# Kernel optimization log

Hardware: AMD Instinct MI355X
Metric: run time of the kernel (lower is better)

Reference implementation:

```python
import jax, jax.numpy as jnp
import numpy as np

N_NODES = 100000
N_EDGES = 1600000
N_GRAPHS = 256
F_NODE, F_EDGE, HID, OUT = 64, 16, 128, 128
BN_SCALE = 1.0 / np.sqrt(1.0 + 1e-5)  # BatchNorm eval with running mean 0, var 1


def setup_inputs() -> dict:
    key = jax.random.key(0)
    ks = iter(jax.random.split(key, 64))
    inp = {}
    inp["x"] = jax.random.normal(next(ks), (N_NODES, F_NODE), dtype=jnp.float32)
    inp["edge_attr"] = jax.random.normal(next(ks), (N_EDGES, F_EDGE), dtype=jnp.float32)
    inp["edge_index"] = jax.random.randint(next(ks), (2, N_EDGES), 0, N_NODES)
    inp["batch"] = jnp.sort(jax.random.randint(next(ks), (N_NODES,), 0, N_GRAPHS))

    def p(shape, scale):
        return (jax.random.normal(next(ks), shape, dtype=jnp.float32) * scale)

    in_dims = [F_NODE, HID, HID]
    for i, d in enumerate(in_dims):
        inp[f"el_w{i}"] = p((F_EDGE, d), F_EDGE ** -0.5)
        inp[f"el_b{i}"] = jnp.zeros((d,), jnp.float32)
        inp[f"c{i}_w1"] = p((d, HID), d ** -0.5)
        inp[f"c{i}_b1"] = jnp.zeros((HID,), jnp.float32)
        inp[f"c{i}_g"] = jnp.ones((HID,), jnp.float32)
        inp[f"c{i}_bt"] = jnp.zeros((HID,), jnp.float32)
        inp[f"c{i}_w2"] = p((HID, HID), HID ** -0.5)
        inp[f"c{i}_b2"] = jnp.zeros((HID,), jnp.float32)
    inp["o_w1"] = p((HID, OUT), HID ** -0.5)
    inp["o_b1"] = jnp.zeros((OUT,), jnp.float32)
    inp["o_w2"] = p((OUT, OUT), OUT ** -0.5)
    inp["o_b2"] = jnp.zeros((OUT,), jnp.float32)
    return inp


def reference(x, edge_attr,
              el_w0, el_b0, c0_w1, c0_b1, c0_g, c0_bt, c0_w2, c0_b2,
              el_w1, el_b1, c1_w1, c1_b1, c1_g, c1_bt, c1_w2, c1_b2,
              el_w2, el_b2, c2_w1, c2_b1, c2_g, c2_bt, c2_w2, c2_b2,
              o_w1, o_b1, o_w2, o_b2,
              edge_index, batch):
    src, dst = edge_index[0], edge_index[1]
    n = x.shape[0]
    layers = [
        (el_w0, el_b0, c0_w1, c0_b1, c0_g, c0_bt, c0_w2, c0_b2),
        (el_w1, el_b1, c1_w1, c1_b1, c1_g, c1_bt, c1_w2, c1_b2),
        (el_w2, el_b2, c2_w1, c2_b1, c2_g, c2_bt, c2_w2, c2_b2),
    ]
    h = x
    for (ew, eb, w1, b1, g, bt, w2, b2) in layers:
        ea = edge_attr @ ew + eb                              # [E, d]
        msg = jax.nn.relu(h[src] + ea)                        # GINEConv message
        agg = jax.ops.segment_sum(msg, dst, num_segments=n)   # scatter-sum to targets
        hh = h + agg                                          # (1+eps)*x + aggr, eps=0
        hh = hh @ w1 + b1                                     # MLP: Linear
        hh = g * (hh * BN_SCALE) + bt                         # BatchNorm1d (eval)
        hh = jax.nn.relu(hh)
        hh = hh @ w2 + b2                                     # MLP: Linear
        h = jax.nn.relu(hh)                                   # dropout(p=0, eval) + act
    s = jax.ops.segment_sum(h, batch, num_segments=N_GRAPHS)
    cnt = jax.ops.segment_sum(jnp.ones((n,), h.dtype), batch, num_segments=N_GRAPHS)
    pooled = s / jnp.maximum(cnt, 1.0)[:, None]               # scatter-mean pooling
    out = jax.nn.relu(pooled @ o_w1 + o_b1) @ o_w2 + o_b2     # out_lin
    return out
```

## Files before the change

### kernel.cpp

```cpp
#include <hip/hip_runtime.h>
#include <hip/hip_fp16.h>
#include <cstdint>
#include <cstddef>

#define N_NODES_C  100000
#define N_EDGES_C  1600000
#define N_GRAPHS_C 256
#define HID_C      128
#define BN_SCALE_C 0.9999950000374997f

#define SCAN_B 1024
#define SCAN_NB ((N_NODES_C + SCAN_B - 1) / SCAN_B)

typedef _Float16 h8 __attribute__((ext_vector_type(8)));
typedef _Float16 h4 __attribute__((ext_vector_type(4)));
typedef float    f4 __attribute__((ext_vector_type(4)));

struct __align__(16) H8 { __half2 v[4]; };
struct __align__(8)  Hq { __half2 a, b; };

__global__ __launch_bounds__(256) void hist_kernel(
    const int* __restrict__ dst, int* __restrict__ counts, int n_edges)
{
    int e = blockIdx.x * 256 + threadIdx.x;
    if (e < n_edges) atomicAdd(&counts[dst[e]], 1);
}

__global__ __launch_bounds__(SCAN_B) void scan1_kernel(
    const int* __restrict__ counts, int* __restrict__ incl,
    int* __restrict__ blocksums, int n)
{
    __shared__ int sdata[SCAN_B];
    const int lid = threadIdx.x;
    const int i = blockIdx.x * SCAN_B + lid;
    sdata[lid] = (i < n) ? counts[i] : 0;
    __syncthreads();
#pragma unroll
    for (int off = 1; off < SCAN_B; off <<= 1) {
        int t = (lid >= off) ? sdata[lid - off] : 0;
        __syncthreads();
        sdata[lid] += t;
        __syncthreads();
    }
    if (i < n) incl[i] = sdata[lid];
    if (lid == SCAN_B - 1) blocksums[blockIdx.x] = sdata[lid];
}

__global__ void scan2_kernel(const int* __restrict__ blocksums,
                             int* __restrict__ blockoffs, int nb)
{
    if (threadIdx.x == 0 && blockIdx.x == 0) {
        int off = 0;
        for (int b = 0; b < nb; ++b) { blockoffs[b] = off; off += blocksums[b]; }
    }
}

__global__ __launch_bounds__(SCAN_B) void scan3_kernel(
    int* __restrict__ incl, const int* __restrict__ blockoffs, int n)
{
    const int i = blockIdx.x * SCAN_B + threadIdx.x;
    if (i < n) incl[i] += blockoffs[blockIdx.x];
}

__global__ __launch_bounds__(256) void initrows_kernel(
    const int* __restrict__ incl, const int* __restrict__ counts,
    int* __restrict__ rowstart, int* __restrict__ cursor, int n)
{
    const int i = blockIdx.x * 256 + threadIdx.x;
    if (i < n) {
        const int rs = incl[i] - counts[i];
        rowstart[i] = rs;
        cursor[i]   = rs;
    }
}

__global__ __launch_bounds__(256) void scatter_kernel(
    const int* __restrict__ src, const int* __restrict__ dst,
    int* __restrict__ cursor, int* __restrict__ perm_src,
    int* __restrict__ perm_eid, int n_edges)
{
    const int e = blockIdx.x * 256 + threadIdx.x;
    if (e < n_edges) {
        const int pos = atomicAdd(&cursor[dst[e]], 1);
        perm_src[pos] = src[e];
        perm_eid[pos] = e;
    }
}

__global__ __launch_bounds__(256) void permute_ea_f16_kernel(
    const float* __restrict__ edge_attr, const int* __restrict__ perm_eid,
    __half* __restrict__ ea_f16, int n_edges)
{
    const int j = blockIdx.x * 256 + threadIdx.x;
    if (j >= n_edges) return;
    const int eid = perm_eid[j];
    const float4* p = (const float4*)(edge_attr + (size_t)eid * 16);
    const float4 q0 = p[0], q1 = p[1], q2 = p[2], q3 = p[3];
    H8 a, b;
    a.v[0] = __floats2half2_rn(q0.x, q0.y);
    a.v[1] = __floats2half2_rn(q0.z, q0.w);
    a.v[2] = __floats2half2_rn(q1.x, q1.y);
    a.v[3] = __floats2half2_rn(q1.z, q1.w);
    b.v[0] = __floats2half2_rn(q2.x, q2.y);
    b.v[1] = __floats2half2_rn(q2.z, q2.w);
    b.v[2] = __floats2half2_rn(q3.x, q3.y);
    b.v[3] = __floats2half2_rn(q3.z, q3.w);
    H8* o = (H8*)(ea_f16 + (size_t)j * 16);
    o[0] = a;
    o[1] = b;
}

__global__ __launch_bounds__(256) void cast_f16_kernel(
    const float* __restrict__ in, _Float16* __restrict__ out, int n4)
{
    const int i = blockIdx.x * 256 + threadIdx.x;
    if (i >= n4) return;
    const float4 v = ((const float4*)in)[i];
    h4 o; o[0] = (_Float16)v.x; o[1] = (_Float16)v.y;
    o[2] = (_Float16)v.z; o[3] = (_Float16)v.w;
    *(h4*)(out + (size_t)i * 4) = o;
}

__global__ __launch_bounds__(256) void transpose_w_kernel(
    const float* __restrict__ w, _Float16* __restrict__ wt, int K, int N)
{
    const int i = blockIdx.x * 256 + threadIdx.x;
    if (i >= K * N) return;
    const int n = i / K;
    const int k = i - n * K;
    wt[(size_t)n * K + k] = (_Float16)w[(size_t)k * N + n];
}

__device__ __forceinline__ float4 eamlp_f16(const H8* __restrict__ p,
                                            const __half2 (*ew2)[4],
                                            const float4 ebv)
{
    const H8 a = p[0], b = p[1];
    __half2 c0 = {0.f, 0.f}, c1 = {0.f, 0.f}, c2 = {0.f, 0.f}, c3 = {0.f, 0.f};
#pragma unroll
    for (int k2 = 0; k2 < 4; ++k2) {
        c0 = __hfma2(a.v[k2], ew2[k2][0], c0);
        c1 = __hfma2(a.v[k2], ew2[k2][1], c1);
        c2 = __hfma2(a.v[k2], ew2[k2][2], c2);
        c3 = __hfma2(a.v[k2], ew2[k2][3], c3);
    }
#pragma unroll
    for (int k2 = 0; k2 < 4; ++k2) {
        c0 = __hfma2(b.v[k2], ew2[4 + k2][0], c0);
        c1 = __hfma2(b.v[k2], ew2[4 + k2][1], c1);
        c2 = __hfma2(b.v[k2], ew2[4 + k2][2], c2);
        c3 = __hfma2(b.v[k2], ew2[4 + k2][3], c3);
    }
    float4 m;
    m.x = ebv.x + __low2float(c0) + __high2float(c0);
    m.y = ebv.y + __low2float(c1) + __high2float(c1);
    m.z = ebv.z + __low2float(c2) + __high2float(c2);
    m.w = ebv.w + __low2float(c3) + __high2float(c3);
    return m;
}

template<int DIN>
__global__ __launch_bounds__(256) void gine_agg_kernel(
    const __half* __restrict__ h16, const __half* __restrict__ ea_f16,
    const int* __restrict__ perm_src,
    const int* __restrict__ rowstart, const int* __restrict__ rowend,
    const float* __restrict__ ew, const float* __restrict__ eb,
    float* __restrict__ agg, int n_nodes)
{
    constexpr int NQ    = DIN / 4;
    constexpr int SLOTS = 256 / NQ;
    const int fq   = threadIdx.x & (NQ - 1);
    const int slot = threadIdx.x / NQ;
    const int v = blockIdx.x * SLOTS + slot;
    if (v >= n_nodes) return;

    __half2 ew2[8][4];
#pragma unroll
    for (int k2 = 0; k2 < 8; ++k2)
#pragma unroll
        for (int fi = 0; fi < 4; ++fi)
            ew2[k2][fi] = __floats2half2_rn(ew[(size_t)(2 * k2)     * DIN + fq * 4 + fi],
                                            ew[(size_t)(2 * k2 + 1) * DIN + fq * 4 + fi]);
    const float4 ebv = *(const float4*)(eb + fq * 4);

    const int s0 = rowstart[v];
    const int s1 = rowend[v];

    float4 acc = {0.f, 0.f, 0.f, 0.f};
    int j = s0;
    for (; j + 2 <= s1; j += 2) {
        const int sn0 = perm_src[j + 0];
        const int sn1 = perm_src[j + 1];
        const Hq hq0 = *(const Hq*)(h16 + (size_t)sn0 * DIN + fq * 4);
        const Hq hq1 = *(const Hq*)(h16 + (size_t)sn1 * DIN + fq * 4);
        const H8* p0 = (const H8*)(ea_f16 + (size_t)(j + 0) * 16);
        const H8* p1 = (const H8*)(ea_f16 + (size_t)(j + 1) * 16);
        const float4 m0 = eamlp_f16(p0, ew2, ebv);
        const float4 m1 = eamlp_f16(p1, ew2, ebv);
        const float2 l0 = __half22float2(hq0.a), u0 = __half22float2(hq0.b);
        const float2 l1 = __half22float2(hq1.a), u1 = __half22float2(hq1.b);
        acc.x += fmaxf(m0.x + l0.x, 0.f) + fmaxf(m1.x + l1.x, 0.f);
        acc.y += fmaxf(m0.y + l0.y, 0.f) + fmaxf(m1.y + l1.y, 0.f);
        acc.z += fmaxf(m0.z + u0.x, 0.f) + fmaxf(m1.z + u1.x, 0.f);
        acc.w += fmaxf(m0.w + u0.y, 0.f) + fmaxf(m1.w + u1.y, 0.f);
    }
    if (j < s1) {
        const int sn = perm_src[j];
        const Hq hq = *(const Hq*)(h16 + (size_t)sn * DIN + fq * 4);
        const H8* p = (const H8*)(ea_f16 + (size_t)j * 16);
        const float4 m = eamlp_f16(p, ew2, ebv);
        const float2 l = __half22float2(hq.a), u = __half22float2(hq.b);
        acc.x += fmaxf(m.x + l.x, 0.f);
        acc.y += fmaxf(m.y + l.y, 0.f);
        acc.z += fmaxf(m.z + u.x, 0.f);
        acc.w += fmaxf(m.w + u.y, 0.f);
    }
    *(float4*)(agg + (size_t)v * DIN + fq * 4) = acc;
}

template<int DIN>
__global__ __launch_bounds__(256) void node_mfma_kernel(
    const float* __restrict__ h, const float* __restrict__ agg,
    const _Float16* __restrict__ w1t, const float* __restrict__ b1,
    const float* __restrict__ gm, const float* __restrict__ bt,
    const _Float16* __restrict__ w2t, const float* __restrict__ b2,
    float* __restrict__ hout, _Float16* __restrict__ h16out, int n_tiles)
{
    constexpr int SXP = DIN + 8;
    constexpr int STP = HID_C + 8;
    __shared__ _Float16 s_x[4][16][SXP];
    __shared__ _Float16 s_t[4][16][STP];

    const int w    = threadIdx.x >> 6;
    const int lane = threadIdx.x & 63;
    int tile = blockIdx.x * 4 + w;
    if (tile >= n_tiles) tile = n_tiles - 1;
    const int node0 = tile * 16;

    constexpr int KQ = DIN / 4;
    for (int it = lane; it < 16 * KQ; it += 64) {
        const int ni = it / KQ;
        const int k4 = (it - ni * KQ) * 4;
        const float4 hv = *(const float4*)(h   + (size_t)(node0 + ni) * DIN + k4);
        const float4 av = *(const float4*)(agg + (size_t)(node0 + ni) * DIN + k4);
        h4 o;
        o[0] = (_Float16)(hv.x + av.x);
        o[1] = (_Float16)(hv.y + av.y);
        o[2] = (_Float16)(hv.z + av.z);
        o[3] = (_Float16)(hv.w + av.w);
        *(h4*)&s_x[w][ni][k4] = o;
    }
    __syncthreads();

    const int ln   = lane & 15;
    const int quad = lane >> 4;

#pragma unroll
    for (int nt = 0; nt < 8; ++nt) {
        const int col = nt * 16 + ln;
        const float bv = b1[col];
        f4 acc = {bv, bv, bv, bv};
#pragma unroll
        for (int ks = 0; ks < DIN / 32; ++ks) {
            const h8 af = *(const h8*)&s_x[w][ln][ks * 32 + quad * 8];
            const h8 bf = *(const h8*)(w1t + (size_t)col * DIN + ks * 32 + quad * 8);
            acc = __builtin_amdgcn_mfma_f32_16x16x32_f16(af, bf, acc, 0, 0, 0);
        }
        const float gv = gm[col], btv = bt[col];
#pragma unroll
        for (int r = 0; r < 4; ++r) {
            const float t = fmaxf(fmaf(acc[r] * BN_SCALE_C, gv, btv), 0.f);
            s_t[w][quad * 4 + r][col] = (_Float16)t;
        }
    }
    __syncthreads();

#pragma unroll
    for (int nt = 0; nt < 8; ++nt) {
        const int col = nt * 16 + ln;
        const float bv = b2[col];
        f4 acc = {bv, bv, bv, bv};
#pragma unroll
        for (int ks = 0; ks < HID_C / 32; ++ks) {
            const h8 af = *(const h8*)&s_t[w][ln][ks * 32 + quad * 8];
            const h8 bf = *(const h8*)(w2t + (size_t)col * HID_C + ks * 32 + quad * 8);
            acc = __builtin_amdgcn_mfma_f32_16x16x32_f16(af, bf, acc, 0, 0, 0);
        }
#pragma unroll
        for (int r = 0; r < 4; ++r) {
            const int node = node0 + quad * 4 + r;
            const float v = fmaxf(acc[r], 0.f);
            hout[(size_t)node * HID_C + col] = v;
            h16out[(size_t)node * HID_C + col] = (_Float16)v;
        }
    }
}

__global__ __launch_bounds__(256) void pool_kernel(
    const float* __restrict__ hfin, const int* __restrict__ batch,
    const float* __restrict__ w1, const float* __restrict__ b1,
    const float* __restrict__ w2, const float* __restrict__ b2,
    float* __restrict__ out, int n_nodes)
{
    const int gid = blockIdx.x;

    int lo = 0, hi = n_nodes;
    while (lo < hi) { int mid = (lo + hi) >> 1; if (batch[mid] < gid) lo = mid + 1; else hi = mid; }
    const int start = lo;
    hi = n_nodes;
    while (lo < hi) { int mid = (lo + hi) >> 1; if (batch[mid] < gid + 1) lo = mid + 1; else hi = mid; }
    const int end = lo;

    const int f = threadIdx.x & (HID_C - 1);
    const int half = threadIdx.x >> 7;

    float sum = 0.f;
    for (int n = start + half; n < end; n += 2)
        sum += hfin[(size_t)n * HID_C + f];

    __shared__ float s_sum[2][HID_C];
    __shared__ float s_p[HID_C];
    __shared__ float s_t[HID_C];
    s_sum[half][f] = sum;
    __syncthreads();

    if (threadIdx.x < HID_C) {
        const float cnt = (float)(end - start);
        s_p[f] = (s_sum[0][f] + s_sum[1][f]) / fmaxf(cnt, 1.f);
    }
    __syncthreads();

    if (threadIdx.x < HID_C) {
        float acc = b1[f];
        for (int k = 0; k < HID_C; ++k) acc = fmaf(s_p[k], w1[k * HID_C + f], acc);
        s_t[f] = fmaxf(acc, 0.f);
    }
    __syncthreads();

    if (threadIdx.x < HID_C) {
        float acc = b2[f];
        for (int k = 0; k < HID_C; ++k) acc = fmaf(s_t[k], w2[k * HID_C + f], acc);
        out[(size_t)gid * HID_C + f] = acc;
    }
}

extern "C" void kernel_launch(void* const* d_in, const int* in_sizes, int n_in,
                              void* d_out, int out_size, void* d_ws, size_t ws_size,
                              hipStream_t stream)
{
    const float* x         = (const float*)d_in[0];
    const float* edge_attr = (const float*)d_in[1];
    const int*   edge_index= (const int*)  d_in[2];
    const int*   batch     = (const int*)  d_in[3];
    const int*   src = edge_index;
    const int*   dst = edge_index + N_EDGES_C;

    const float* el_w[3] = {(const float*)d_in[4],  (const float*)d_in[12], (const float*)d_in[20]};
    const float* el_b[3] = {(const float*)d_in[5],  (const float*)d_in[13], (const float*)d_in[21]};
    const float* c_w1[3] = {(const float*)d_in[6],  (const float*)d_in[14], (const float*)d_in[22]};
    const float* c_b1[3] = {(const float*)d_in[7],  (const float*)d_in[15], (const float*)d_in[23]};
    const float* c_g [3] = {(const float*)d_in[8],  (const float*)d_in[16], (const float*)d_in[24]};
    const float* c_bt[3] = {(const float*)d_in[9],  (const float*)d_in[17], (const float*)d_in[25]};
    const float* c_w2[3] = {(const float*)d_in[10], (const float*)d_in[18], (const float*)d_in[26]};
    const float* c_b2[3] = {(const float*)d_in[11], (const float*)d_in[19], (const float*)d_in[27]};
    const float* o_w1 = (const float*)d_in[28];
    const float* o_b1 = (const float*)d_in[29];
    const float* o_w2 = (const float*)d_in[30];
    const float* o_b2 = (const float*)d_in[31];

    char* wsp = (char*)d_ws;
    size_t used = 0;
    auto alloc = [&](size_t bytes) { char* p = wsp + used; used += (bytes + 255) & ~(size_t)255; return p; };
    float* h        = (float*)alloc((size_t)N_NODES_C * HID_C * 4);
    float* agg      = (float*)alloc((size_t)N_NODES_C * HID_C * 4);
    int*   counts   = (int*)alloc((size_t)N_NODES_C * 4);
    int*   incl     = (int*)alloc((size_t)N_NODES_C * 4);
    int*   rowstart = (int*)alloc((size_t)N_NODES_C * 4);
    int*   cursor   = (int*)alloc((size_t)N_NODES_C * 4);
    int*   blocksums= (int*)alloc(128 * 4);
    int*   blockoffs= (int*)alloc(128 * 4);
    int*   perm_src = (int*)alloc((size_t)N_EDGES_C * 4);
    int*   perm_eid = (int*)alloc((size_t)N_EDGES_C * 4);
    __half*    ea_f16 = (__half*)alloc((size_t)N_EDGES_C * 16 * 2);
    _Float16*  h_f16  = (_Float16*)alloc((size_t)N_NODES_C * HID_C * 2);
    _Float16*  x_f16  = (_Float16*)alloc((size_t)N_NODES_C * 64 * 2);
    _Float16*  w1t[3], *w2t[3];
    for (int l = 0; l < 3; ++l) {
        w1t[l] = (_Float16*)alloc((size_t)HID_C * HID_C * 2);
        w2t[l] = (_Float16*)alloc((size_t)HID_C * HID_C * 2);
    }
    (void)ws_size;

    hipMemsetAsync(counts, 0, (size_t)N_NODES_C * 4, stream);
    hist_kernel<<<(N_EDGES_C + 255) / 256, 256, 0, stream>>>(dst, counts, N_EDGES_C);
    scan1_kernel<<<SCAN_NB, SCAN_B, 0, stream>>>(counts, incl, blocksums, N_NODES_C);
    scan2_kernel<<<1, 64, 0, stream>>>(blocksums, blockoffs, SCAN_NB);
    scan3_kernel<<<SCAN_NB, SCAN_B, 0, stream>>>(incl, blockoffs, N_NODES_C);
    initrows_kernel<<<(N_NODES_C + 255) / 256, 256, 0, stream>>>(incl, counts, rowstart,
                                                                 cursor, N_NODES_C);
    scatter_kernel<<<(N_EDGES_C + 255) / 256, 256, 0, stream>>>(src, dst, cursor,
                                                                perm_src, perm_eid, N_EDGES_C);
    permute_ea_f16_kernel<<<(N_EDGES_C + 255) / 256, 256, 0, stream>>>(
        edge_attr, perm_eid, ea_f16, N_EDGES_C);
    cast_f16_kernel<<<(N_NODES_C * 64 / 4 + 255) / 256, 256, 0, stream>>>(
        x, x_f16, N_NODES_C * 64 / 4);
    for (int l = 0; l < 3; ++l) {
        const int K1 = (l == 0) ? 64 : HID_C;
        transpose_w_kernel<<<(K1 * HID_C + 255) / 256, 256, 0, stream>>>(
            c_w1[l], w1t[l], K1, HID_C);
        transpose_w_kernel<<<(HID_C * HID_C + 255) / 256, 256, 0, stream>>>(
            c_w2[l], w2t[l], HID_C, HID_C);
    }

    const int n_tiles = N_NODES_C / 16;
    const int nb_node = (n_tiles + 3) / 4;

    for (int l = 0; l < 3; ++l) {
        if (l == 0) {
            gine_agg_kernel<64><<<(N_NODES_C + 15) / 16, 256, 0, stream>>>(
                (const __half*)x_f16, ea_f16, perm_src, rowstart, incl,
                el_w[0], el_b[0], agg, N_NODES_C);
            node_mfma_kernel<64><<<nb_node, 256, 0, stream>>>(
                x, agg, w1t[0], c_b1[0], c_g[0], c_bt[0], w2t[0], c_b2[0],
                h, h_f16, n_tiles);
        } else {
            gine_agg_kernel<128><<<(N_NODES_C + 7) / 8, 256, 0, stream>>>(
                (const __half*)h_f16, ea_f16, perm_src, rowstart, incl,
                el_w[l], el_b[l], agg, N_NODES_C);
            node_mfma_kernel<128><<<nb_node, 256, 0, stream>>>(
                h, agg, w1t[l], c_b1[l], c_g[l], c_bt[l], w2t[l], c_b2[l],
                h, h_f16, n_tiles);
        }
    }

    pool_kernel<<<N_GRAPHS_C, 256, 0, stream>>>(h, batch, o_w1, o_b1, o_w2, o_b2,
                                                (float*)d_out, N_NODES_C);
}
```

Measured before the change: 1.104 ms.

## Fuse edge-attr permute into scatter, drop fp32 node state, half-precision edge MLP

```diff
diff --git a/kernel.cpp b/kernel.cpp
--- a/kernel.cpp
+++ b/kernel.cpp
@@ -14,10 +14,9 @@
 
 typedef _Float16 h8 __attribute__((ext_vector_type(8)));
 typedef _Float16 h4 __attribute__((ext_vector_type(4)));
+typedef _Float16 hv2 __attribute__((ext_vector_type(2)));
 typedef float    f4 __attribute__((ext_vector_type(4)));
-
-struct __align__(16) H8 { __half2 v[4]; };
-struct __align__(8)  Hq { __half2 a, b; };
+typedef float    f2 __attribute__((ext_vector_type(2)));
 
 __global__ __launch_bounds__(256) void hist_kernel(
     const int* __restrict__ dst, int* __restrict__ counts, int n_edges)
@@ -74,38 +73,28 @@
     }
 }
 
-__global__ __launch_bounds__(256) void scatter_kernel(
+__global__ __launch_bounds__(256) void scatter_fused_kernel(
     const int* __restrict__ src, const int* __restrict__ dst,
+    const float* __restrict__ edge_attr,
     int* __restrict__ cursor, int* __restrict__ perm_src,
-    int* __restrict__ perm_eid, int n_edges)
+    _Float16* __restrict__ ea_f16, int n_edges)
 {
     const int e = blockIdx.x * 256 + threadIdx.x;
-    if (e < n_edges) {
-        const int pos = atomicAdd(&cursor[dst[e]], 1);
-        perm_src[pos] = src[e];
-        perm_eid[pos] = e;
-    }
-}
-
-__global__ __launch_bounds__(256) void permute_ea_f16_kernel(
-    const float* __restrict__ edge_attr, const int* __restrict__ perm_eid,
-    __half* __restrict__ ea_f16, int n_edges)
-{
-    const int j = blockIdx.x * 256 + threadIdx.x;
-    if (j >= n_edges) return;
-    const int eid = perm_eid[j];
-    const float4* p = (const float4*)(edge_attr + (size_t)eid * 16);
+    if (e >= n_edges) return;
+    const int pos = atomicAdd(&cursor[dst[e]], 1);
+    perm_src[pos] = src[e];
+    const float4* p = (const float4*)(edge_attr + (size_t)e * 16);
     const float4 q0 = p[0], q1 = p[1], q2 = p[2], q3 = p[3];
-    H8 a, b;
-    a.v[0] = __floats2half2_rn(q0.x, q0.y);
-    a.v[1] = __floats2half2_rn(q0.z, q0.w);
-    a.v[2] = __floats2half2_rn(q1.x, q1.y);
-    a.v[3] = __floats2half2_rn(q1.z, q1.w);
-    b.v[0] = __floats2half2_rn(q2.x, q2.y);
-    b.v[1] = __floats2half2_rn(q2.z, q2.w);
-    b.v[2] = __floats2half2_rn(q3.x, q3.y);
-    b.v[3] = __floats2half2_rn(q3.z, q3.w);
-    H8* o = (H8*)(ea_f16 + (size_t)j * 16);
+    h8 a, b;
+    a[0] = (_Float16)q0.x; a[1] = (_Float16)q0.y;
+    a[2] = (_Float16)q0.z; a[3] = (_Float16)q0.w;
+    a[4] = (_Float16)q1.x; a[5] = (_Float16)q1.y;
+    a[6] = (_Float16)q1.z; a[7] = (_Float16)q1.w;
+    b[0] = (_Float16)q2.x; b[1] = (_Float16)q2.y;
+    b[2] = (_Float16)q2.z; b[3] = (_Float16)q2.w;
+    b[4] = (_Float16)q3.x; b[5] = (_Float16)q3.y;
+    b[6] = (_Float16)q3.z; b[7] = (_Float16)q3.w;
+    h8* o = (h8*)(ea_f16 + (size_t)pos * 16);
     o[0] = a;
     o[1] = b;
 }
@@ -131,37 +120,9 @@
     wt[(size_t)n * K + k] = (_Float16)w[(size_t)k * N + n];
 }
 
-__device__ __forceinline__ float4 eamlp_f16(const H8* __restrict__ p,
-                                            const __half2 (*ew2)[4],
-                                            const float4 ebv)
-{
-    const H8 a = p[0], b = p[1];
-    __half2 c0 = {0.f, 0.f}, c1 = {0.f, 0.f}, c2 = {0.f, 0.f}, c3 = {0.f, 0.f};
-#pragma unroll
-    for (int k2 = 0; k2 < 4; ++k2) {
-        c0 = __hfma2(a.v[k2], ew2[k2][0], c0);
-        c1 = __hfma2(a.v[k2], ew2[k2][1], c1);
-        c2 = __hfma2(a.v[k2], ew2[k2][2], c2);
-        c3 = __hfma2(a.v[k2], ew2[k2][3], c3);
-    }
-#pragma unroll
-    for (int k2 = 0; k2 < 4; ++k2) {
-        c0 = __hfma2(b.v[k2], ew2[4 + k2][0], c0);
-        c1 = __hfma2(b.v[k2], ew2[4 + k2][1], c1);
-        c2 = __hfma2(b.v[k2], ew2[4 + k2][2], c2);
-        c3 = __hfma2(b.v[k2], ew2[4 + k2][3], c3);
-    }
-    float4 m;
-    m.x = ebv.x + __low2float(c0) + __high2float(c0);
-    m.y = ebv.y + __low2float(c1) + __high2float(c1);
-    m.z = ebv.z + __low2float(c2) + __high2float(c2);
-    m.w = ebv.w + __low2float(c3) + __high2float(c3);
-    return m;
-}
-
 template<int DIN>
 __global__ __launch_bounds__(256) void gine_agg_kernel(
-    const __half* __restrict__ h16, const __half* __restrict__ ea_f16,
+    const _Float16* __restrict__ h16, const _Float16* __restrict__ ea_f16,
     const int* __restrict__ perm_src,
     const int* __restrict__ rowstart, const int* __restrict__ rowend,
     const float* __restrict__ ew, const float* __restrict__ eb,
@@ -174,57 +135,103 @@
     const int v = blockIdx.x * SLOTS + slot;
     if (v >= n_nodes) return;
 
-    __half2 ew2[8][4];
-#pragma unroll
-    for (int k2 = 0; k2 < 8; ++k2)
-#pragma unroll
-        for (int fi = 0; fi < 4; ++fi)
-            ew2[k2][fi] = __floats2half2_rn(ew[(size_t)(2 * k2)     * DIN + fq * 4 + fi],
-                                            ew[(size_t)(2 * k2 + 1) * DIN + fq * 4 + fi]);
-    const float4 ebv = *(const float4*)(eb + fq * 4);
+    hv2 ew01[16], ew23[16];
+#pragma unroll
+    for (int k = 0; k < 16; ++k) {
+        const float* wr = ew + (size_t)k * DIN + fq * 4;
+        ew01[k][0] = (_Float16)wr[0]; ew01[k][1] = (_Float16)wr[1];
+        ew23[k][0] = (_Float16)wr[2]; ew23[k][1] = (_Float16)wr[3];
+    }
+    hv2 eb01, eb23;
+    {
+        const float4 ebv = *(const float4*)(eb + fq * 4);
+        eb01[0] = (_Float16)ebv.x; eb01[1] = (_Float16)ebv.y;
+        eb23[0] = (_Float16)ebv.z; eb23[1] = (_Float16)ebv.w;
+    }
+    const hv2 zz = {(_Float16)0.f, (_Float16)0.f};
 
     const int s0 = rowstart[v];
     const int s1 = rowend[v];
 
-    float4 acc = {0.f, 0.f, 0.f, 0.f};
+    f4 acc = {0.f, 0.f, 0.f, 0.f};
     int j = s0;
     for (; j + 2 <= s1; j += 2) {
         const int sn0 = perm_src[j + 0];
         const int sn1 = perm_src[j + 1];
-        const Hq hq0 = *(const Hq*)(h16 + (size_t)sn0 * DIN + fq * 4);
-        const Hq hq1 = *(const Hq*)(h16 + (size_t)sn1 * DIN + fq * 4);
-        const H8* p0 = (const H8*)(ea_f16 + (size_t)(j + 0) * 16);
-        const H8* p1 = (const H8*)(ea_f16 + (size_t)(j + 1) * 16);
-        const float4 m0 = eamlp_f16(p0, ew2, ebv);
-        const float4 m1 = eamlp_f16(p1, ew2, ebv);
-        const float2 l0 = __half22float2(hq0.a), u0 = __half22float2(hq0.b);
-        const float2 l1 = __half22float2(hq1.a), u1 = __half22float2(hq1.b);
-        acc.x += fmaxf(m0.x + l0.x, 0.f) + fmaxf(m1.x + l1.x, 0.f);
-        acc.y += fmaxf(m0.y + l0.y, 0.f) + fmaxf(m1.y + l1.y, 0.f);
-        acc.z += fmaxf(m0.z + u0.x, 0.f) + fmaxf(m1.z + u1.x, 0.f);
-        acc.w += fmaxf(m0.w + u0.y, 0.f) + fmaxf(m1.w + u1.y, 0.f);
+        const h4 hq0 = *(const h4*)(h16 + (size_t)sn0 * DIN + fq * 4);
+        const h4 hq1 = *(const h4*)(h16 + (size_t)sn1 * DIN + fq * 4);
+        const h8* p0 = (const h8*)(ea_f16 + (size_t)(j + 0) * 16);
+        const h8* p1 = (const h8*)(ea_f16 + (size_t)(j + 1) * 16);
+        const h8 a0 = p0[0], a1 = p0[1];
+        const h8 b0 = p1[0], b1 = p1[1];
+
+        hv2 c01 = eb01, c23 = eb23;
+        hv2 d01 = eb01, d23 = eb23;
+#pragma unroll
+        for (int k = 0; k < 8; ++k) {
+            const hv2 ba = {a0[k], a0[k]};
+            const hv2 bb = {b0[k], b0[k]};
+            c01 += ba * ew01[k];  c23 += ba * ew23[k];
+            d01 += bb * ew01[k];  d23 += bb * ew23[k];
+        }
+#pragma unroll
+        for (int k = 0; k < 8; ++k) {
+            const hv2 ba = {a1[k], a1[k]};
+            const hv2 bb = {b1[k], b1[k]};
+            c01 += ba * ew01[8 + k];  c23 += ba * ew23[8 + k];
+            d01 += bb * ew01[8 + k];  d23 += bb * ew23[8 + k];
+        }
+        const hv2 h001 = {hq0[0], hq0[1]}, h023 = {hq0[2], hq0[3]};
+        const hv2 h101 = {hq1[0], hq1[1]}, h123 = {hq1[2], hq1[3]};
+        c01 = __builtin_elementwise_max(c01 + h001, zz);
+        c23 = __builtin_elementwise_max(c23 + h023, zz);
+        d01 = __builtin_elementwise_max(d01 + h101, zz);
+        d23 = __builtin_elementwise_max(d23 + h123, zz);
+        const f2 r0 = __builtin_convertvector(c01, f2);
+        const f2 r1 = __builtin_convertvector(c23, f2);
+        const f2 r2 = __builtin_convertvector(d01, f2);
+        const f2 r3 = __builtin_convertvector(d23, f2);
+        acc[0] += r0[0] + r2[0];
+        acc[1] += r0[1] + r2[1];
+        acc[2] += r1[0] + r3[0];
+        acc[3] += r1[1] + r3[1];
     }
     if (j < s1) {
         const int sn = perm_src[j];
-        const Hq hq = *(const Hq*)(h16 + (size_t)sn * DIN + fq * 4);
-        const H8* p = (const H8*)(ea_f16 + (size_t)j * 16);
-        const float4 m = eamlp_f16(p, ew2, ebv);
-        const float2 l = __half22float2(hq.a), u = __half22float2(hq.b);
-        acc.x += fmaxf(m.x + l.x, 0.f);
-        acc.y += fmaxf(m.y + l.y, 0.f);
-        acc.z += fmaxf(m.z + u.x, 0.f);
-        acc.w += fmaxf(m.w + u.y, 0.f);
-    }
-    *(float4*)(agg + (size_t)v * DIN + fq * 4) = acc;
+        const h4 hq = *(const h4*)(h16 + (size_t)sn * DIN + fq * 4);
+        const h8* p = (const h8*)(ea_f16 + (size_t)j * 16);
+        const h8 a0 = p[0], a1 = p[1];
+        hv2 c01 = eb01, c23 = eb23;
+#pragma unroll
+        for (int k = 0; k < 8; ++k) {
+            const hv2 ba = {a0[k], a0[k]};
+            c01 += ba * ew01[k];  c23 += ba * ew23[k];
+        }
+#pragma unroll
+        for (int k = 0; k < 8; ++k) {
+            const hv2 ba = {a1[k], a1[k]};
+            c01 += ba * ew01[8 + k];  c23 += ba * ew23[8 + k];
+        }
+        const hv2 h01 = {hq[0], hq[1]}, h23 = {hq[2], hq[3]};
+        c01 = __builtin_elementwise_max(c01 + h01, zz);
+        c23 = __builtin_elementwise_max(c23 + h23, zz);
+        const f2 r0 = __builtin_convertvector(c01, f2);
+        const f2 r1 = __builtin_convertvector(c23, f2);
+        acc[0] += r0[0];
+        acc[1] += r0[1];
+        acc[2] += r1[0];
+        acc[3] += r1[1];
+    }
+    *(f4*)(agg + (size_t)v * DIN + fq * 4) = acc;
 }
 
 template<int DIN>
 __global__ __launch_bounds__(256) void node_mfma_kernel(
-    const float* __restrict__ h, const float* __restrict__ agg,
+    const _Float16* __restrict__ hin16, const float* __restrict__ agg,
     const _Float16* __restrict__ w1t, const float* __restrict__ b1,
     const float* __restrict__ gm, const float* __restrict__ bt,
     const _Float16* __restrict__ w2t, const float* __restrict__ b2,
-    float* __restrict__ hout, _Float16* __restrict__ h16out, int n_tiles)
+    _Float16* __restrict__ h16out, int n_tiles)
 {
     constexpr int SXP = DIN + 8;
     constexpr int STP = HID_C + 8;
@@ -241,13 +248,13 @@
     for (int it = lane; it < 16 * KQ; it += 64) {
         const int ni = it / KQ;
         const int k4 = (it - ni * KQ) * 4;
-        const float4 hv = *(const float4*)(h   + (size_t)(node0 + ni) * DIN + k4);
+        const h4 hv = *(const h4*)(hin16 + (size_t)(node0 + ni) * DIN + k4);
         const float4 av = *(const float4*)(agg + (size_t)(node0 + ni) * DIN + k4);
         h4 o;
-        o[0] = (_Float16)(hv.x + av.x);
-        o[1] = (_Float16)(hv.y + av.y);
-        o[2] = (_Float16)(hv.z + av.z);
-        o[3] = (_Float16)(hv.w + av.w);
+        o[0] = (_Float16)((float)hv[0] + av.x);
+        o[1] = (_Float16)((float)hv[1] + av.y);
+        o[2] = (_Float16)((float)hv[2] + av.z);
+        o[3] = (_Float16)((float)hv[3] + av.w);
         *(h4*)&s_x[w][ni][k4] = o;
     }
     __syncthreads();
@@ -289,15 +296,13 @@
 #pragma unroll
         for (int r = 0; r < 4; ++r) {
             const int node = node0 + quad * 4 + r;
-            const float v = fmaxf(acc[r], 0.f);
-            hout[(size_t)node * HID_C + col] = v;
-            h16out[(size_t)node * HID_C + col] = (_Float16)v;
+            h16out[(size_t)node * HID_C + col] = (_Float16)fmaxf(acc[r], 0.f);
         }
     }
 }
 
 __global__ __launch_bounds__(256) void pool_kernel(
-    const float* __restrict__ hfin, const int* __restrict__ batch,
+    const _Float16* __restrict__ hfin, const int* __restrict__ batch,
     const float* __restrict__ w1, const float* __restrict__ b1,
     const float* __restrict__ w2, const float* __restrict__ b2,
     float* __restrict__ out, int n_nodes)
@@ -316,7 +321,7 @@
 
     float sum = 0.f;
     for (int n = start + half; n < end; n += 2)
-        sum += hfin[(size_t)n * HID_C + f];
+        sum += (float)hfin[(size_t)n * HID_C + f];
 
     __shared__ float s_sum[2][HID_C];
     __shared__ float s_p[HID_C];
@@ -371,7 +376,6 @@
     char* wsp = (char*)d_ws;
     size_t used = 0;
     auto alloc = [&](size_t bytes) { char* p = wsp + used; used += (bytes + 255) & ~(size_t)255; return p; };
-    float* h        = (float*)alloc((size_t)N_NODES_C * HID_C * 4);
     float* agg      = (float*)alloc((size_t)N_NODES_C * HID_C * 4);
     int*   counts   = (int*)alloc((size_t)N_NODES_C * 4);
     int*   incl     = (int*)alloc((size_t)N_NODES_C * 4);
@@ -380,11 +384,10 @@
     int*   blocksums= (int*)alloc(128 * 4);
     int*   blockoffs= (int*)alloc(128 * 4);
     int*   perm_src = (int*)alloc((size_t)N_EDGES_C * 4);
-    int*   perm_eid = (int*)alloc((size_t)N_EDGES_C * 4);
-    __half*    ea_f16 = (__half*)alloc((size_t)N_EDGES_C * 16 * 2);
-    _Float16*  h_f16  = (_Float16*)alloc((size_t)N_NODES_C * HID_C * 2);
-    _Float16*  x_f16  = (_Float16*)alloc((size_t)N_NODES_C * 64 * 2);
-    _Float16*  w1t[3], *w2t[3];
+    _Float16* ea_f16 = (_Float16*)alloc((size_t)N_EDGES_C * 16 * 2);
+    _Float16* h_f16  = (_Float16*)alloc((size_t)N_NODES_C * HID_C * 2);
+    _Float16* x_f16  = (_Float16*)alloc((size_t)N_NODES_C * 64 * 2);
+    _Float16* w1t[3], *w2t[3];
     for (int l = 0; l < 3; ++l) {
         w1t[l] = (_Float16*)alloc((size_t)HID_C * HID_C * 2);
         w2t[l] = (_Float16*)alloc((size_t)HID_C * HID_C * 2);
@@ -398,10 +401,8 @@
     scan3_kernel<<<SCAN_NB, SCAN_B, 0, stream>>>(incl, blockoffs, N_NODES_C);
     initrows_kernel<<<(N_NODES_C + 255) / 256, 256, 0, stream>>>(incl, counts, rowstart,
                                                                  cursor, N_NODES_C);
-    scatter_kernel<<<(N_EDGES_C + 255) / 256, 256, 0, stream>>>(src, dst, cursor,
-                                                                perm_src, perm_eid, N_EDGES_C);
-    permute_ea_f16_kernel<<<(N_EDGES_C + 255) / 256, 256, 0, stream>>>(
-        edge_attr, perm_eid, ea_f16, N_EDGES_C);
+    scatter_fused_kernel<<<(N_EDGES_C + 255) / 256, 256, 0, stream>>>(
+        src, dst, edge_attr, cursor, perm_src, ea_f16, N_EDGES_C);
     cast_f16_kernel<<<(N_NODES_C * 64 / 4 + 255) / 256, 256, 0, stream>>>(
         x, x_f16, N_NODES_C * 64 / 4);
     for (int l = 0; l < 3; ++l) {
@@ -418,21 +419,21 @@
     for (int l = 0; l < 3; ++l) {
         if (l == 0) {
             gine_agg_kernel<64><<<(N_NODES_C + 15) / 16, 256, 0, stream>>>(
-                (const __half*)x_f16, ea_f16, perm_src, rowstart, incl,
+                x_f16, ea_f16, perm_src, rowstart, incl,
                 el_w[0], el_b[0], agg, N_NODES_C);
             node_mfma_kernel<64><<<nb_node, 256, 0, stream>>>(
-                x, agg, w1t[0], c_b1[0], c_g[0], c_bt[0], w2t[0], c_b2[0],
-                h, h_f16, n_tiles);
+                x_f16, agg, w1t[0], c_b1[0], c_g[0], c_bt[0], w2t[0], c_b2[0],
+                h_f16, n_tiles);
         } else {
             gine_agg_kernel<128><<<(N_NODES_C + 7) / 8, 256, 0, stream>>>(
-                (const __half*)h_f16, ea_f16, perm_src, rowstart, incl,
+                h_f16, ea_f16, perm_src, rowstart, incl,
                 el_w[l], el_b[l], agg, N_NODES_C);
             node_mfma_kernel<128><<<nb_node, 256, 0, stream>>>(
-                h, agg, w1t[l], c_b1[l], c_g[l], c_bt[l], w2t[l], c_b2[l],
-                h, h_f16, n_tiles);
-        }
-    }
-
-    pool_kernel<<<N_GRAPHS_C, 256, 0, stream>>>(h, batch, o_w1, o_b1, o_w2, o_b2,
+                h_f16, agg, w1t[l], c_b1[l], c_g[l], c_bt[l], w2t[l], c_b2[l],
+                h_f16, n_tiles);
+        }
+    }
+
+    pool_kernel<<<N_GRAPHS_C, 256, 0, stream>>>(h_f16, batch, o_w1, o_b1, o_w2, o_b2,
                                                 (float*)d_out, N_NODES_C);
 }
```

Measured after the change: 1.180 ms. 1.07x slower.
